# Kernel tuning notes

Hardware: AMD Instinct MI355X
Metric: run time of the kernel (lower is better)

The kernel has to match this reference:

```python
import jax, jax.numpy as jnp
import numpy as np

N_NODES = 50000
N_EDGES = 800000
D_FEAT = 128
EMBED = 128
HEADS = 8
HEAD_DIM = EMBED // HEADS


def setup_inputs() -> dict:
    key = jax.random.key(0)
    ks = jax.random.split(key, 10)
    xavier = jax.nn.initializers.xavier_normal()
    return {
        "nodes": jax.random.normal(ks[0], (N_NODES, D_FEAT), jnp.float32),
        "edges": jax.random.normal(ks[1], (N_EDGES, D_FEAT), jnp.float32),
        "senders": jax.random.randint(ks[2], (N_EDGES,), 0, N_NODES, jnp.int32),
        "receivers": jax.random.randint(ks[3], (N_EDGES,), 0, N_NODES, jnp.int32),
        "Ws_k": xavier(ks[4], (D_FEAT, EMBED), jnp.float32),
        "Ws_b": jnp.zeros((EMBED,), jnp.float32),
        "Wr_k": xavier(ks[5], (D_FEAT, EMBED), jnp.float32),
        "Wr_b": jnp.zeros((EMBED,), jnp.float32),
        "We_k": xavier(ks[6], (D_FEAT, EMBED), jnp.float32),
        "We_b": jnp.zeros((EMBED,), jnp.float32),
        "a": xavier(ks[7], (HEADS, HEAD_DIM), jnp.float32),
    }


def reference(nodes, edges, senders, receivers, Ws_k, Ws_b, Wr_k, Wr_b, We_k, We_b, a):
    N = nodes.shape[0]
    E = edges.shape[0]
    H, D = a.shape
    # Node-level projections (linear, so equivalent to projecting gathered edge endpoints)
    hs = nodes @ Ws_k + Ws_b            # [N, HD]  (W_s on sent attributes)
    hr = nodes @ Wr_k + Wr_b            # [N, HD]  (W_r on received attributes)
    he = edges @ We_k + We_b            # [E, HD]  (W_e on edge attributes)
    sent = hs[senders]                  # [E, HD]
    x = jax.nn.leaky_relu(sent + hr[receivers] + he)  # default slope 0.01, as original
    xh = x.reshape(E, H, D)
    logits = jnp.sum(xh * a, axis=-1)   # [E, H]
    # segment_softmax over receivers (stable: subtract per-segment max)
    mx = jax.ops.segment_max(logits, receivers, num_segments=N)  # [N, H]
    mx = jnp.where(jnp.isfinite(mx), mx, 0.0)
    ex = jnp.exp(logits - mx[receivers])                         # [E, H]
    denom = jax.ops.segment_sum(ex, receivers, num_segments=N)   # [N, H]
    w = ex / denom[receivers]                                    # [E, H]
    msg = (w[..., None] * sent.reshape(E, H, D)).reshape(E, H * D)
    out = jax.ops.segment_sum(msg, receivers, num_segments=N)    # [N, HD]
    return out
```

## Files before the change

kernel.cpp:

```cpp
#include <hip/hip_runtime.h>

#define N_NODES 50000
#define N_EDGES 800000
#define D 128
#define HEADS 8

typedef __attribute__((ext_vector_type(8))) short short8b;
typedef __attribute__((ext_vector_type(4))) float f32x4;

__device__ __forceinline__ unsigned short f2bf_rne(float f) {
    unsigned int u = __float_as_uint(f);
    u += 0x7FFFu + ((u >> 16) & 1u);
    return (unsigned short)(u >> 16);
}
__device__ __forceinline__ float bf2f(unsigned short u) {
    return __uint_as_float(((unsigned int)u) << 16);
}

#define K1_ROWS 128
__global__ __launch_bounds__(256, 3) void k_node_proj_mfma(
    const float* __restrict__ nodes,
    const float* __restrict__ Ws, const float* __restrict__ bs,
    const float* __restrict__ Wr, const float* __restrict__ br,
    unsigned short* __restrict__ hsb, unsigned short* __restrict__ hrb)
{
    __shared__ __align__(16) unsigned short WT[D][136];
    __shared__ __align__(16) unsigned short At[64][136];
    const int ntiles = (N_NODES + K1_ROWS - 1) / K1_ROWS;
    int bx = blockIdx.x;
    int proj = (bx >= ntiles) ? 1 : 0;
    int tile = proj ? (bx - ntiles) : bx;
    const float* W    = proj ? Wr : Ws;
    const float* bias = proj ? br : bs;
    unsigned short* outp = proj ? hrb : hsb;
    int t = threadIdx.x;
    int lane = t & 63;
    int wv = t >> 6;
    int lg = lane >> 4;
    int li = lane & 15;

    #pragma unroll 8
    for (int j = 0; j < 64; ++j) {
        int idx = t + 256 * j;
        int k = idx >> 7, c = idx & 127;
        WT[c][k] = f2bf_rne(W[idx]);
    }
    float b_ct[8];
    #pragma unroll
    for (int ct = 0; ct < 8; ++ct) b_ct[ct] = bias[ct * 16 + li];

    #pragma unroll 1
    for (int sub = 0; sub < 2; ++sub) {
        int row0 = tile * K1_ROWS + sub * 64;
        if (row0 >= N_NODES) break;
        __syncthreads();
        {
            const float4* Nv = (const float4*)nodes;
            #pragma unroll
            for (int j = 0; j < 8; ++j) {
                int fi = t + 256 * j;
                int r = row0 + (fi >> 5);
                float4 v = make_float4(0.f, 0.f, 0.f, 0.f);
                if (r < N_NODES) v = Nv[(size_t)r * 32 + (fi & 31)];
                ushort4 b;
                b.x = f2bf_rne(v.x); b.y = f2bf_rne(v.y);
                b.z = f2bf_rne(v.z); b.w = f2bf_rne(v.w);
                *(ushort4*)&At[fi >> 5][(fi & 31) * 4] = b;
            }
        }
        __syncthreads();

        short8b afr[4];
        #pragma unroll
        for (int kb = 0; kb < 4; ++kb)
            afr[kb] = *(const short8b*)&At[wv * 16 + li][kb * 32 + lg * 8];

        #pragma unroll
        for (int ct = 0; ct < 8; ++ct) {
            f32x4 acc = {0.f, 0.f, 0.f, 0.f};
            #pragma unroll
            for (int kb = 0; kb < 4; ++kb) {
                short8b bfr = *(const short8b*)&WT[ct * 16 + li][kb * 32 + lg * 8];
                acc = __builtin_amdgcn_mfma_f32_16x16x32_bf16(afr[kb], bfr, acc, 0, 0, 0);
            }
            #pragma unroll
            for (int j = 0; j < 4; ++j) {
                int r = row0 + wv * 16 + lg * 4 + j;
                if (r < N_NODES)
                    outp[(size_t)r * D + ct * 16 + li] = f2bf_rne(acc[j] + b_ct[ct]);
            }
        }
    }
}

__global__ __launch_bounds__(256) void k_hist(
    const int* __restrict__ receivers, int* __restrict__ deg)
{
    int i = blockIdx.x * 256 + threadIdx.x;
    if (i < N_EDGES) atomicAdd(&deg[receivers[i]], 1);
}

#define SCAN_CHUNK 49
__global__ __launch_bounds__(1024) void k_scan(
    const int* __restrict__ deg, int* __restrict__ rowptr, int* __restrict__ cursor)
{
    __shared__ int sm[1024];
    int t = threadIdx.x;
    int base = t * SCAN_CHUNK;
    int lsum = 0;
    #pragma unroll 4
    for (int i = 0; i < SCAN_CHUNK; ++i) {
        int idx = base + i;
        if (idx < N_NODES) lsum += deg[idx];
    }
    sm[t] = lsum;
    __syncthreads();
    for (int off = 1; off < 1024; off <<= 1) {
        int v = (t >= off) ? sm[t - off] : 0;
        __syncthreads();
        sm[t] += v;
        __syncthreads();
    }
    int run = (t > 0) ? sm[t - 1] : 0;
    for (int i = 0; i < SCAN_CHUNK; ++i) {
        int idx = base + i;
        if (idx < N_NODES) {
            rowptr[idx] = run;
            cursor[idx] = run;
            run += deg[idx];
        }
    }
    if (t == 1023) rowptr[N_NODES] = sm[1023];
}

__global__ __launch_bounds__(256) void k_fill(
    const int* __restrict__ receivers, const int* __restrict__ senders,
    int* __restrict__ cursor,
    int* __restrict__ eids, int* __restrict__ s_csr, int* __restrict__ r_csr)
{
    int i = blockIdx.x * 256 + threadIdx.x;
    if (i < N_EDGES) {
        int r = receivers[i];
        int pos = atomicAdd(&cursor[r], 1);
        eids[pos]  = i;
        s_csr[pos] = senders[i];
        r_csr[pos] = r;
    }
}

#define BLK_E 64
__global__ __launch_bounds__(256, 3) void k_edge_logits_mfma(
    const float* __restrict__ edges,
    const int* __restrict__ eids, const int* __restrict__ s_csr,
    const int* __restrict__ r_csr,
    const float* __restrict__ We, const float* __restrict__ be,
    const float* __restrict__ a,
    const unsigned short* __restrict__ hsb, const unsigned short* __restrict__ hrb,
    float* __restrict__ ex)
{
    __shared__ __align__(16) unsigned short WeT[D][136];
    __shared__ __align__(16) unsigned short Et[BLK_E][136];
    int t = threadIdx.x;
    int lane = t & 63;
    int wv = t >> 6;
    int lg = lane >> 4;
    int li = lane & 15;

    #pragma unroll 8
    for (int j = 0; j < 64; ++j) {
        int idx = t + 256 * j;
        int k = idx >> 7, c = idx & 127;
        WeT[c][k] = f2bf_rne(We[idx]);
    }
    float a_h[HEADS], be_h[HEADS];
    #pragma unroll
    for (int h = 0; h < HEADS; ++h) {
        a_h[h]  = a[h * 16 + li];
        be_h[h] = be[h * 16 + li];
    }
    int jm = li & 3;
    __syncthreads();

    const int ntiles = N_EDGES / BLK_E;
    for (int tile = blockIdx.x; tile < ntiles; tile += gridDim.x) {
        int pbase = tile * BLK_E + wv * 16;

        {
            const float4* Ev = (const float4*)edges;
            #pragma unroll
            for (int j = 0; j < 8; ++j) {
                int fi = lane + 64 * j;
                int rloc = fi >> 5;
                int e = eids[pbase + rloc];
                float4 v = Ev[(size_t)e * 32 + (fi & 31)];
                ushort4 b;
                b.x = f2bf_rne(v.x); b.y = f2bf_rne(v.y);
                b.z = f2bf_rne(v.z); b.w = f2bf_rne(v.w);
                *(ushort4*)&Et[wv * 16 + rloc][(fi & 31) * 4] = b;
            }
        }

        int sj[4], rj[4];
        #pragma unroll
        for (int j = 0; j < 4; ++j) {
            sj[j] = s_csr[pbase + lg * 4 + j];
            rj[j] = r_csr[pbase + lg * 4 + j];
        }
        unsigned short g_hs[4][HEADS], g_hr[4][HEADS];
        #pragma unroll
        for (int j = 0; j < 4; ++j) {
            const unsigned short* hsrow = hsb + (size_t)sj[j] * D + li;
            const unsigned short* hrrow = hrb + (size_t)rj[j] * D + li;
            #pragma unroll
            for (int h = 0; h < HEADS; ++h) {
                g_hs[j][h] = hsrow[h * 16];
                g_hr[j][h] = hrrow[h * 16];
            }
        }

        asm volatile("s_waitcnt lgkmcnt(0)" ::: "memory");
        __builtin_amdgcn_sched_barrier(0);

        short8b afr[4];
        #pragma unroll
        for (int kb = 0; kb < 4; ++kb)
            afr[kb] = *(const short8b*)&Et[wv * 16 + li][kb * 32 + lg * 8];

        #pragma unroll
        for (int h = 0; h < HEADS; ++h) {
            f32x4 acc = {0.f, 0.f, 0.f, 0.f};
            #pragma unroll
            for (int kb = 0; kb < 4; ++kb) {
                short8b bfr = *(const short8b*)&WeT[h * 16 + li][kb * 32 + lg * 8];
                acc = __builtin_amdgcn_mfma_f32_16x16x32_bf16(afr[kb], bfr, acc, 0, 0, 0);
            }
            float p[4];
            #pragma unroll
            for (int j = 0; j < 4; ++j) {
                float x = acc[j] + be_h[h] + bf2f(g_hs[j][h]) + bf2f(g_hr[j][h]);
                x = x > 0.f ? x : 0.01f * x;
                p[j] = x * a_h[h];
            }
            #pragma unroll
            for (int j = 0; j < 4; ++j) {
                p[j] += __shfl_xor(p[j], 1);
                p[j] += __shfl_xor(p[j], 2);
            }
            float q = (jm & 1) ? ((jm & 2) ? p[3] : p[1])
                               : ((jm & 2) ? p[2] : p[0]);
            q += __shfl_xor(q, 4);
            q += __shfl_xor(q, 8);
            float e_ = __expf(q);
            if (li < 4) {
                int pos = pbase + lg * 4 + li;
                ex[(size_t)pos * HEADS + h] = e_;
            }
        }
        __builtin_amdgcn_wave_barrier();
    }
}

__global__ __launch_bounds__(256) void k_gather_out(
    const int* __restrict__ rowptr, const int* __restrict__ s_csr,
    const unsigned short* __restrict__ hsb, const float* __restrict__ ex,
    float* __restrict__ out)
{
    int r = blockIdx.x * 4 + (threadIdx.x >> 6);
    int l = threadIdx.x & 63;
    int h = l >> 3;
    int beg = rowptr[r], end = rowptr[r + 1];

    float2 acc = make_float2(0.f, 0.f);
    float dsum = 0.f;
    for (int j0 = beg; j0 < end; j0 += 16) {
        int cnt = end - j0;
        int s[16]; float w[16];
        #pragma unroll
        for (int q = 0; q < 16; ++q)
            if (q < cnt) { s[q] = s_csr[j0 + q]; w[q] = ex[(size_t)(j0 + q) * HEADS + h]; }
        #pragma unroll
        for (int q = 0; q < 16; ++q)
            if (q < cnt) {
                ushort2 hv = *(const ushort2*)&hsb[(size_t)s[q] * D + 2 * l];
                acc.x += w[q] * bf2f(hv.x);
                acc.y += w[q] * bf2f(hv.y);
                dsum  += w[q];
            }
    }
    float inv = (end > beg && dsum != 0.f) ? (1.0f / dsum) : 0.f;
    acc.x *= inv; acc.y *= inv;
    *(float2*)&out[(size_t)r * D + 2 * l] = acc;
}

extern "C" void kernel_launch(void* const* d_in, const int* in_sizes, int n_in,
                              void* d_out, int out_size, void* d_ws, size_t ws_size,
                              hipStream_t stream) {
    const float* nodes     = (const float*)d_in[0];
    const float* edges     = (const float*)d_in[1];
    const int*   senders   = (const int*)d_in[2];
    const int*   receivers = (const int*)d_in[3];
    const float* Ws = (const float*)d_in[4];
    const float* bs = (const float*)d_in[5];
    const float* Wr = (const float*)d_in[6];
    const float* br = (const float*)d_in[7];
    const float* We = (const float*)d_in[8];
    const float* be = (const float*)d_in[9];
    const float* a  = (const float*)d_in[10];
    float* out = (float*)d_out;

    unsigned short* hsb = (unsigned short*)d_ws;
    unsigned short* hrb = hsb + (size_t)N_NODES * D;
    float* ex   = (float*)(hrb + (size_t)N_NODES * D);
    int* deg    = (int*)(ex + (size_t)N_EDGES * HEADS);
    int* rowptr = deg + N_NODES;
    int* cursor = rowptr + N_NODES + 1;
    int* eids   = cursor + N_NODES;
    int* s_csr  = eids + N_EDGES;
    int* r_csr  = s_csr + N_EDGES;

    (void)hipMemsetAsync(deg, 0, N_NODES * sizeof(int), stream);
    k_hist<<<N_EDGES / 256, 256, 0, stream>>>(receivers, deg);
    k_scan<<<1, 1024, 0, stream>>>(deg, rowptr, cursor);
    k_fill<<<N_EDGES / 256, 256, 0, stream>>>(receivers, senders, cursor,
                                              eids, s_csr, r_csr);
    int ntiles_n = (N_NODES + K1_ROWS - 1) / K1_ROWS;
    k_node_proj_mfma<<<ntiles_n * 2, 256, 0, stream>>>(nodes, Ws, bs, Wr, br, hsb, hrb);
    k_edge_logits_mfma<<<2500, 256, 0, stream>>>(edges, eids, s_csr, r_csr,
                                                 We, be, a, hsb, hrb, ex);
    k_gather_out<<<N_NODES / 4, 256, 0, stream>>>(rowptr, s_csr, hsb, ex, out);
}
```

Measured before the change: 460.7 us.

## Read edges in original order and scatter logits to CSR positions

The edge-logit kernel now streams the edge feature rows contiguously in original edge order, with coalesced loads, instead of gathering them through a CSR permutation. The fill kernel records each edge's CSR position so the per-edge exp-logits can be scattered to that slot as one float2 store per lane. The eids and r_csr arrays are dropped, and the cross-lane head reductions use DPP row adds instead of shuffles. The trade is a scattered 32-byte write per edge in place of the large gathered 512-byte edge-row reads.

```diff
diff --git a/kernel.cpp b/kernel.cpp
--- a/kernel.cpp
+++ b/kernel.cpp
@@ -15,6 +15,19 @@
 }
 __device__ __forceinline__ float bf2f(unsigned short u) {
     return __uint_as_float(((unsigned int)u) << 16);
+}
+
+template <int CTRL>
+__device__ __forceinline__ float dpp_radd(float v) {
+    int s = __builtin_amdgcn_update_dpp(0, __float_as_int(v), CTRL, 0xF, 0xF, true);
+    return v + __int_as_float(s);
+}
+__device__ __forceinline__ float rowsum16(float v) {
+    v = dpp_radd<0xB1>(v);
+    v = dpp_radd<0x4E>(v);
+    v = dpp_radd<0x141>(v);
+    v = dpp_radd<0x140>(v);
+    return v;
 }
 
 #define K1_ROWS 128
@@ -136,23 +149,22 @@
 __global__ __launch_bounds__(256) void k_fill(
     const int* __restrict__ receivers, const int* __restrict__ senders,
     int* __restrict__ cursor,
-    int* __restrict__ eids, int* __restrict__ s_csr, int* __restrict__ r_csr)
+    int* __restrict__ s_csr, int* __restrict__ pos_csr)
 {
     int i = blockIdx.x * 256 + threadIdx.x;
     if (i < N_EDGES) {
         int r = receivers[i];
         int pos = atomicAdd(&cursor[r], 1);
-        eids[pos]  = i;
-        s_csr[pos] = senders[i];
-        r_csr[pos] = r;
+        s_csr[pos]  = senders[i];
+        pos_csr[i]  = pos;
     }
 }
 
 #define BLK_E 64
 __global__ __launch_bounds__(256, 3) void k_edge_logits_mfma(
     const float* __restrict__ edges,
-    const int* __restrict__ eids, const int* __restrict__ s_csr,
-    const int* __restrict__ r_csr,
+    const int* __restrict__ senders, const int* __restrict__ receivers,
+    const int* __restrict__ pos_csr,
     const float* __restrict__ We, const float* __restrict__ be,
     const float* __restrict__ a,
     const unsigned short* __restrict__ hsb, const unsigned short* __restrict__ hrb,
@@ -178,34 +190,34 @@
         a_h[h]  = a[h * 16 + li];
         be_h[h] = be[h * 16 + li];
     }
-    int jm = li & 3;
     __syncthreads();
 
     const int ntiles = N_EDGES / BLK_E;
+    const float4* Ev = (const float4*)edges;
+
     for (int tile = blockIdx.x; tile < ntiles; tile += gridDim.x) {
-        int pbase = tile * BLK_E + wv * 16;
-
-        {
-            const float4* Ev = (const float4*)edges;
-            #pragma unroll
-            for (int j = 0; j < 8; ++j) {
-                int fi = lane + 64 * j;
-                int rloc = fi >> 5;
-                int e = eids[pbase + rloc];
-                float4 v = Ev[(size_t)e * 32 + (fi & 31)];
-                ushort4 b;
-                b.x = f2bf_rne(v.x); b.y = f2bf_rne(v.y);
-                b.z = f2bf_rne(v.z); b.w = f2bf_rne(v.w);
-                *(ushort4*)&Et[wv * 16 + rloc][(fi & 31) * 4] = b;
-            }
+        int pb = tile * BLK_E + wv * 16;
+
+        #pragma unroll
+        for (int j = 0; j < 8; ++j) {
+            int fi = lane + 64 * j;
+            int rloc = fi >> 5;
+            float4 v = Ev[(size_t)(pb + rloc) * 32 + (fi & 31)];
+            ushort4 b;
+            b.x = f2bf_rne(v.x); b.y = f2bf_rne(v.y);
+            b.z = f2bf_rne(v.z); b.w = f2bf_rne(v.w);
+            *(ushort4*)&Et[wv * 16 + rloc][(fi & 31) * 4] = b;
         }
 
         int sj[4], rj[4];
         #pragma unroll
         for (int j = 0; j < 4; ++j) {
-            sj[j] = s_csr[pbase + lg * 4 + j];
-            rj[j] = r_csr[pbase + lg * 4 + j];
-        }
+            sj[j] = senders[pb + lg * 4 + j];
+            rj[j] = receivers[pb + lg * 4 + j];
+        }
+        int o = 4 * lg + (li >> 2);
+        int mypos = pos_csr[pb + o];
+
         unsigned short g_hs[4][HEADS], g_hr[4][HEADS];
         #pragma unroll
         for (int j = 0; j < 4; ++j) {
@@ -226,6 +238,7 @@
         for (int kb = 0; kb < 4; ++kb)
             afr[kb] = *(const short8b*)&Et[wv * 16 + li][kb * 32 + lg * 8];
 
+        float hold[8];
         #pragma unroll
         for (int h = 0; h < HEADS; ++h) {
             f32x4 acc = {0.f, 0.f, 0.f, 0.f};
@@ -234,27 +247,26 @@
                 short8b bfr = *(const short8b*)&WeT[h * 16 + li][kb * 32 + lg * 8];
                 acc = __builtin_amdgcn_mfma_f32_16x16x32_bf16(afr[kb], bfr, acc, 0, 0, 0);
             }
-            float p[4];
+            float pr[4];
             #pragma unroll
             for (int j = 0; j < 4; ++j) {
                 float x = acc[j] + be_h[h] + bf2f(g_hs[j][h]) + bf2f(g_hr[j][h]);
-                x = x > 0.f ? x : 0.01f * x;
-                p[j] = x * a_h[h];
-            }
-            #pragma unroll
-            for (int j = 0; j < 4; ++j) {
-                p[j] += __shfl_xor(p[j], 1);
-                p[j] += __shfl_xor(p[j], 2);
-            }
-            float q = (jm & 1) ? ((jm & 2) ? p[3] : p[1])
-                               : ((jm & 2) ? p[2] : p[0]);
-            q += __shfl_xor(q, 4);
-            q += __shfl_xor(q, 8);
-            float e_ = __expf(q);
-            if (li < 4) {
-                int pos = pbase + lg * 4 + li;
-                ex[(size_t)pos * HEADS + h] = e_;
-            }
+                x = fmaxf(x, 0.01f * x);
+                pr[j] = rowsum16(x * a_h[h]);
+            }
+            float qa = (li & 4) ? pr[1] : pr[0];
+            float qb = (li & 4) ? pr[3] : pr[2];
+            hold[h] = __expf((li & 8) ? qb : qa);
+        }
+        {
+            float a0 = (li & 1) ? hold[2] : hold[0];
+            float a1 = (li & 1) ? hold[6] : hold[4];
+            float ea = (li & 2) ? a1 : a0;
+            float b0 = (li & 1) ? hold[3] : hold[1];
+            float b1 = (li & 1) ? hold[7] : hold[5];
+            float eb = (li & 2) ? b1 : b0;
+            int h1 = 2 * (li & 3);
+            *(float2*)&ex[(size_t)mypos * HEADS + h1] = make_float2(ea, eb);
         }
         __builtin_amdgcn_wave_barrier();
     }
@@ -310,22 +322,21 @@
 
     unsigned short* hsb = (unsigned short*)d_ws;
     unsigned short* hrb = hsb + (size_t)N_NODES * D;
-    float* ex   = (float*)(hrb + (size_t)N_NODES * D);
-    int* deg    = (int*)(ex + (size_t)N_EDGES * HEADS);
-    int* rowptr = deg + N_NODES;
-    int* cursor = rowptr + N_NODES + 1;
-    int* eids   = cursor + N_NODES;
-    int* s_csr  = eids + N_EDGES;
-    int* r_csr  = s_csr + N_EDGES;
+    float* ex    = (float*)(hrb + (size_t)N_NODES * D);
+    int* deg     = (int*)(ex + (size_t)N_EDGES * HEADS);
+    int* rowptr  = deg + N_NODES;
+    int* cursor  = rowptr + N_NODES + 1;
+    int* s_csr   = cursor + N_NODES;
+    int* pos_csr = s_csr + N_EDGES;
 
     (void)hipMemsetAsync(deg, 0, N_NODES * sizeof(int), stream);
     k_hist<<<N_EDGES / 256, 256, 0, stream>>>(receivers, deg);
     k_scan<<<1, 1024, 0, stream>>>(deg, rowptr, cursor);
     k_fill<<<N_EDGES / 256, 256, 0, stream>>>(receivers, senders, cursor,
-                                              eids, s_csr, r_csr);
+                                              s_csr, pos_csr);
     int ntiles_n = (N_NODES + K1_ROWS - 1) / K1_ROWS;
     k_node_proj_mfma<<<ntiles_n * 2, 256, 0, stream>>>(nodes, Ws, bs, Wr, br, hsb, hrb);
-    k_edge_logits_mfma<<<2500, 256, 0, stream>>>(edges, eids, s_csr, r_csr,
+    k_edge_logits_mfma<<<2500, 256, 0, stream>>>(edges, senders, receivers, pos_csr,
                                                  We, be, a, hsb, hrb, ex);
     k_gather_out<<<N_NODES / 4, 256, 0, stream>>>(rowptr, s_csr, hsb, ex, out);
 }
```

Result: faster. 444.1 us (-3.6%).
